# Kernel tuning notes

Hardware: AMD Instinct MI355X
Metric: run time of the kernel (lower is better)

The kernel has to match this reference:

```python
import jax, jax.numpy as jnp
import numpy as np

EMBED_DIM = 768
NUM_HEADS = 12
HEAD_DIM = EMBED_DIM // NUM_HEADS
B, T = 2, 2048


def setup_inputs() -> dict:
    key = jax.random.key(0)
    kx, kq, kqb, ko, kob = jax.random.split(key, 5)
    x = jax.random.normal(kx, (B, T, EMBED_DIM), dtype=jnp.float32)
    # xavier-uniform style params
    lim_qkv = float(np.sqrt(6.0 / (EMBED_DIM + 3 * EMBED_DIM)))
    qkv_kernel = jax.random.uniform(kq, (EMBED_DIM, 3 * EMBED_DIM), minval=-lim_qkv, maxval=lim_qkv, dtype=jnp.float32)
    qkv_bias = jnp.zeros((3 * EMBED_DIM,), dtype=jnp.float32)
    lim_o = float(np.sqrt(6.0 / (EMBED_DIM + EMBED_DIM)))
    o_kernel = jax.random.uniform(ko, (EMBED_DIM, EMBED_DIM), minval=-lim_o, maxval=lim_o, dtype=jnp.float32)
    o_bias = jnp.zeros((EMBED_DIM,), dtype=jnp.float32)
    return {"x": x, "qkv_kernel": qkv_kernel, "qkv_bias": qkv_bias, "o_kernel": o_kernel, "o_bias": o_bias}


def reference(x, qkv_kernel, qkv_bias, o_kernel, o_bias):
    b, t, d = x.shape
    # fused QKV projection
    qkv = jnp.einsum('btd,de->bte', x, qkv_kernel) + qkv_bias  # [B,T,3D]
    qkv = qkv.reshape(b, t, 3, NUM_HEADS, HEAD_DIM).transpose(2, 0, 3, 1, 4)  # [3,B,H,T,Dh]
    q, k, v = qkv[0], qkv[1], qkv[2]
    # naive attention: materializes full [B,H,T,T] scores (as in original)
    scale = 1.0 / np.sqrt(HEAD_DIM).astype(np.float32)
    attn_logits = jnp.einsum('bhqd,bhkd->bhqk', q, k) * scale
    attention = jax.nn.softmax(attn_logits, axis=-1)
    values = jnp.einsum('bhqk,bhkd->bhqd', attention, v)
    values = values.transpose(0, 2, 1, 3).reshape(b, t, d)  # [B,T,D]
    o = jnp.einsum('btd,de->bte', values, o_kernel) + o_bias
    return (o, attention)
```

## Files before the change

### kernel.cpp

```cpp
#include <hip/hip_runtime.h>
#include <hip/hip_bf16.h>
#include <hip/hip_fp16.h>

typedef _Float16 f16;
typedef _Float16 f16x4 __attribute__((ext_vector_type(4)));
typedef _Float16 f16x8 __attribute__((ext_vector_type(8)));
typedef float f32x4 __attribute__((ext_vector_type(4)));

#define MFMA16(a, b, c) __builtin_amdgcn_mfma_f32_16x16x32_f16(a, b, c, 0, 0, 0)

__device__ __forceinline__ float fexp2(float x) {
#if __has_builtin(__builtin_amdgcn_exp2f)
    return __builtin_amdgcn_exp2f(x);
#else
    return exp2f(x);
#endif
}

typedef __attribute__((address_space(1))) const void gconst_t;
typedef __attribute__((address_space(3))) void lds_t;
__device__ __forceinline__ void gload16(const f16* g, f16* l) {
    __builtin_amdgcn_global_load_lds((gconst_t*)g, (lds_t*)l, 16, 0, 0);
}

__global__ void k_convert_x(const float* __restrict__ in, f16* __restrict__ out, int n4) {
    int i = blockIdx.x * blockDim.x + threadIdx.x;
    if (i >= n4) return;
    float4 v = ((const float4*)in)[i];
    f16x4 o = {(f16)v.x, (f16)v.y, (f16)v.z, (f16)v.w};
    ((f16x4*)out)[i] = o;
}

__global__ __launch_bounds__(256) void k_transpose(const float* __restrict__ in,
                                                   f16* __restrict__ out, int K, int N) {
    __shared__ f16 tile[64][72];
    int n0 = blockIdx.x * 64, k0 = blockIdx.y * 64;
    int t = threadIdx.x;
    int r = t >> 2, cb = (t & 3) * 16;
    const float* src = in + (size_t)(k0 + r) * N + n0 + cb;
#pragma unroll
    for (int j = 0; j < 4; ++j) {
        float4 v = ((const float4*)src)[j];
        tile[r][cb + 4 * j + 0] = (f16)v.x;
        tile[r][cb + 4 * j + 1] = (f16)v.y;
        tile[r][cb + 4 * j + 2] = (f16)v.z;
        tile[r][cb + 4 * j + 3] = (f16)v.w;
    }
    __syncthreads();
    int nl = t >> 2, kb = (t & 3) * 16;
    f16* dst = out + (size_t)(n0 + nl) * K + k0 + kb;
#pragma unroll
    for (int j = 0; j < 2; ++j) {
        f16x8 o;
#pragma unroll
        for (int e = 0; e < 8; ++e) o[e] = tile[kb + 8 * j + e][nl];
        *(f16x8*)(dst + 8 * j) = o;
    }
}

__device__ __forceinline__ void gemm_core(const f16* __restrict__ A, const f16* __restrict__ Bt,
                                          int m0, int n0, int lane, int w, int wr, int wc,
                                          f16* As, f16* Bs, f32x4 acc[4][4]) {
    int prow = lane >> 2, pc = lane & 3;
    int lrow = prow ^ ((prow >> 2) & 1);
    int lcol = (pc ^ (lrow & 3)) * 8;
    int rsw = (lane & 7) << 3;
    for (int kt = 0; kt < 24; ++kt) {
        const f16* ab = A + (size_t)(m0 + w * 32 + lrow) * 768 + kt * 32 + lcol;
        const f16* bb = Bt + (size_t)(n0 + w * 32 + lrow) * 768 + kt * 32 + lcol;
        gload16(ab, As + (w * 32) * 32);
        gload16(ab + (size_t)16 * 768, As + (w * 32 + 16) * 32);
        gload16(bb, Bs + (w * 32) * 32);
        gload16(bb + (size_t)16 * 768, Bs + (w * 32 + 16) * 32);
        __syncthreads();
        f16x8 a[4], b[4];
#pragma unroll
        for (int i = 0; i < 4; ++i) {
            int idx = (wr * 64 + i * 16 + (lane & 15)) * 32 + (lane >> 4) * 8;
            a[i] = *(const f16x8*)(As + (idx ^ rsw));
        }
#pragma unroll
        for (int j = 0; j < 4; ++j) {
            int idx = (wc * 64 + j * 16 + (lane & 15)) * 32 + (lane >> 4) * 8;
            b[j] = *(const f16x8*)(Bs + (idx ^ rsw));
        }
#pragma unroll
        for (int i = 0; i < 4; ++i)
#pragma unroll
            for (int j = 0; j < 4; ++j) acc[i][j] = MFMA16(a[i], b[j], acc[i][j]);
        __syncthreads();
    }
}

__global__ __launch_bounds__(256) void k_qkv_gemm(const f16* __restrict__ A, const f16* __restrict__ Bt,
                                                  const float* __restrict__ bias,
                                                  f16* __restrict__ Qh, f16* __restrict__ Kf,
                                                  f16* __restrict__ Vf) {
    __shared__ __align__(16) f16 As[128 * 32];
    __shared__ __align__(16) f16 Bs[128 * 32];
    int m0 = blockIdx.x * 128, n0 = blockIdx.y * 128;
    int t = threadIdx.x, lane = t & 63, w = t >> 6;
    int wr = w >> 1, wc = w & 1;
    f32x4 zero = {0.f, 0.f, 0.f, 0.f};
    f32x4 acc[4][4];
#pragma unroll
    for (int i = 0; i < 4; ++i)
#pragma unroll
        for (int j = 0; j < 4; ++j) acc[i][j] = zero;

    gemm_core(A, Bt, m0, n0, lane, w, wr, wc, As, Bs, acc);

    const float QSCALE = 0.18033688011112042f;
#pragma unroll
    for (int j = 0; j < 4; ++j) {
        int n = n0 + wc * 64 + j * 16 + (lane & 15);
        int which = n / 768;
        int rem = n - which * 768;
        int h = rem >> 6, d = rem & 63;
        float bv = bias[n];
#pragma unroll
        for (int i = 0; i < 4; ++i) {
            int m = m0 + wr * 64 + i * 16 + ((lane >> 4) << 2);
            int bb = m >> 11, tt = m & 2047;
            int bh = bb * 12 + h;
            if (which == 2) {
                int kt = tt >> 6;
                int half = (tt & 63) >> 5, hi = (tt & 31) >> 3, e0 = tt & 7;
                int jd = d >> 4, lo = d & 15;
                size_t addr = (((size_t)bh * 32 + kt) * 8 + jd * 2 + half) * 512 +
                              (size_t)(hi * 16 + lo) * 8 + e0;
                f16x4 pk;
#pragma unroll
                for (int r = 0; r < 4; ++r) pk[r] = (f16)(acc[i][j][r] + bv);
                *(f16x4*)(Vf + addr) = pk;
            } else if (which == 0) {
#pragma unroll
                for (int r = 0; r < 4; ++r)
                    Qh[((size_t)bh * 2048 + tt + r) * 64 + d] = (f16)((acc[i][j][r] + bv) * QSCALE);
            } else {
                int half = d >> 5, hi = (d & 31) >> 3, e = d & 7;
#pragma unroll
                for (int r = 0; r < 4; ++r) {
                    int tr = tt + r;
                    int kt = tr >> 6, row = tr & 63;
                    int s = row >> 4, lo = row & 15;
                    size_t addr = (((size_t)bh * 32 + kt) * 8 + s * 2 + half) * 512 +
                                  (size_t)(hi * 16 + lo) * 8 + e;
                    Kf[addr] = (f16)(acc[i][j][r] + bv);
                }
            }
        }
    }
}

__global__ __launch_bounds__(256) void k_o_gemm(const f16* __restrict__ A, const f16* __restrict__ Bt,
                                                const float* __restrict__ bias,
                                                float* __restrict__ out) {
    __shared__ __align__(16) f16 As[128 * 32];
    __shared__ __align__(16) f16 Bs[128 * 32];
    int m0 = blockIdx.x * 128, n0 = blockIdx.y * 128;
    int t = threadIdx.x, lane = t & 63, w = t >> 6;
    int wr = w >> 1, wc = w & 1;
    f32x4 zero = {0.f, 0.f, 0.f, 0.f};
    f32x4 acc[4][4];
#pragma unroll
    for (int i = 0; i < 4; ++i)
#pragma unroll
        for (int j = 0; j < 4; ++j) acc[i][j] = zero;

    gemm_core(A, Bt, m0, n0, lane, w, wr, wc, As, Bs, acc);

#pragma unroll
    for (int j = 0; j < 4; ++j) {
        int n = n0 + wc * 64 + j * 16 + (lane & 15);
        float bv = bias[n];
#pragma unroll
        for (int i = 0; i < 4; ++i) {
            int m = m0 + wr * 64 + i * 16 + ((lane >> 4) << 2);
#pragma unroll
            for (int r = 0; r < 4; ++r) out[(size_t)(m + r) * 768 + n] = acc[i][j][r] + bv;
        }
    }
}

__global__ __launch_bounds__(256) void k_lsum(const f16* __restrict__ Qh, const f16* __restrict__ Kf,
                                              float* __restrict__ lpart) {
    int qt = blockIdx.x, bh = blockIdx.y, kc = blockIdx.z;
    int q0 = qt * 64;
    int t = threadIdx.x, lane = t & 63, w = t >> 6;
    const f16* qbase = Qh + ((size_t)bh * 2048 + q0 + w * 16) * 64;
    const f16* kfb = Kf + (size_t)bh * 32 * 4096 + (size_t)lane * 8;

    f16x8 aq[2];
#pragma unroll
    for (int f = 0; f < 2; ++f)
        aq[f] = *(const f16x8*)(qbase + (size_t)(lane & 15) * 64 + f * 32 + (lane >> 4) * 8);
    f32x4 zero = {0.f, 0.f, 0.f, 0.f};

    auto LOADK = [&](f16x8* dst, int kt) {
        const f16* kp = kfb + (size_t)kt * 4096;
#pragma unroll
        for (int f = 0; f < 8; ++f) dst[f] = *(const f16x8*)(kp + f * 512);
    };
    auto QKTS = [&](const f16x8* kf, f32x4* s4) {
#pragma unroll
        for (int s = 0; s < 4; ++s) {
            s4[s] = MFMA16(kf[2 * s], aq[0], zero);
            s4[s] = MFMA16(kf[2 * s + 1], aq[1], s4[s]);
        }
    };

    f16x8 ka[8], kb2[8];
    float lsum = 0.f;
    int base = kc * 8;
    LOADK(ka, base);
    for (int i = 0; i < 8; i += 2) {
        f32x4 s4[4];
        LOADK(kb2, base + i + 1);
        QKTS(ka, s4);
#pragma unroll
        for (int s = 0; s < 4; ++s)
#pragma unroll
            for (int r = 0; r < 4; ++r) lsum += fexp2(s4[s][r]);
        LOADK(ka, base + ((i + 2) & 7));
        QKTS(kb2, s4);
#pragma unroll
        for (int s = 0; s < 4; ++s)
#pragma unroll
            for (int r = 0; r < 4; ++r) lsum += fexp2(s4[s][r]);
    }
    lsum += __shfl_xor(lsum, 16, 64);
    lsum += __shfl_xor(lsum, 32, 64);
    float* lp = lpart + (size_t)kc * 49152 + (size_t)bh * 2048 + q0 + w * 16;
    if (lane < 16) lp[lane] = lsum;
}

__global__ __launch_bounds__(512, 4) void k_attn(const f16* __restrict__ Qh, const f16* __restrict__ Kf,
                                                 const f16* __restrict__ Vf,
                                                 const float* __restrict__ lpart,
                                                 float* __restrict__ attn, f16* __restrict__ valh) {
    __shared__ __align__(16) float Ps32_all[8][16 * 68];
    int orig = blockIdx.x;
    int swz = (orig & 7) * 96 + (orig >> 3);
    int bh = swz >> 5, qt = swz & 31;
    int q0 = qt * 64;
    int t = threadIdx.x, lane = t & 63, w = t >> 6;
    int qg = w >> 1, half = w & 1;

    const f16* qbase = Qh + ((size_t)bh * 2048 + q0 + qg * 16) * 64;
    const f16* kfb = Kf + (size_t)bh * 32 * 4096 + (size_t)lane * 8;
    const f16* vfb = Vf + (size_t)bh * 32 * 4096 + (size_t)lane * 8;

    f16x8 aq[2];
#pragma unroll
    for (int f = 0; f < 2; ++f)
        aq[f] = *(const f16x8*)(qbase + (size_t)(lane & 15) * 64 + f * 32 + (lane >> 4) * 8);
    f32x4 zero = {0.f, 0.f, 0.f, 0.f};

    float linv;
    {
        size_t qoff = (size_t)bh * 2048 + q0 + qg * 16 + (lane & 15);
        float s = 0.f;
#pragma unroll
        for (int kc = 0; kc < 4; ++kc) s += lpart[(size_t)kc * 49152 + qoff];
        linv = 1.0f / s;
    }

    auto LOADK = [&](f16x8* dst, int kt) {
        const f16* kp = kfb + (size_t)kt * 4096;
#pragma unroll
        for (int f = 0; f < 8; ++f) dst[f] = *(const f16x8*)(kp + f * 512);
    };

    f32x4 accv[4];
#pragma unroll
    for (int j = 0; j < 4; ++j) accv[j] = zero;
    float* Ps = Ps32_all[w];
    float* attn_base = attn + ((size_t)bh * 2048 + q0 + qg * 16) * 2048;
    f16x8 ka[8], vbuf[8];

    int ktbase = half * 16;
    LOADK(ka, ktbase);
    for (int kt = ktbase; kt < ktbase + 16; ++kt) {
        {
            const f16* vp = vfb + (size_t)kt * 4096;
#pragma unroll
            for (int f = 0; f < 8; ++f) vbuf[f] = *(const f16x8*)(vp + f * 512);
        }
        f32x4 s4[4];
#pragma unroll
        for (int s = 0; s < 4; ++s) {
            s4[s] = MFMA16(ka[2 * s], aq[0], zero);
            s4[s] = MFMA16(ka[2 * s + 1], aq[1], s4[s]);
        }
        LOADK(ka, (kt + 1) & 31);
#pragma unroll
        for (int s = 0; s < 4; ++s) {
            f32x4 pv;
#pragma unroll
            for (int r = 0; r < 4; ++r) pv[r] = fexp2(s4[s][r]) * linv;
            *(f32x4*)(Ps + (lane & 15) * 68 + s * 16 + (lane >> 4) * 4) = pv;
        }
        f16x8 pa[2];
#pragma unroll
        for (int hh = 0; hh < 2; ++hh) {
            const float* pr = Ps + (lane & 15) * 68 + hh * 32 + (lane >> 4) * 8;
            f32x4 lo = *(const f32x4*)(pr);
            f32x4 hi = *(const f32x4*)(pr + 4);
            f16x8 pf = {(f16)lo[0], (f16)lo[1], (f16)lo[2], (f16)lo[3],
                        (f16)hi[0], (f16)hi[1], (f16)hi[2], (f16)hi[3]};
            pa[hh] = pf;
        }
        float* ab = attn_base + kt * 64;
#pragma unroll
        for (int i = 0; i < 4; ++i) {
            int row = i * 4 + (lane >> 4);
            int col = (lane & 15) * 4;
            f32x4 v = *(const f32x4*)(Ps + row * 68 + col);
            *(f32x4*)(ab + (size_t)row * 2048 + col) = v;
        }
#pragma unroll
        for (int jd = 0; jd < 4; ++jd) {
            accv[jd] = MFMA16(pa[0], vbuf[2 * jd], accv[jd]);
            accv[jd] = MFMA16(pa[1], vbuf[2 * jd + 1], accv[jd]);
        }
    }

    if (half) {
#pragma unroll
        for (int j = 0; j < 4; ++j)
#pragma unroll
            for (int r = 0; r < 4; ++r)
                Ps[((lane >> 4) * 4 + r) * 68 + j * 16 + (lane & 15)] = accv[j][r];
    }
    __syncthreads();
    if (!half) {
        const float* Pp = Ps32_all[w + 1];
        int b = bh / 12, h = bh - b * 12;
#pragma unroll
        for (int j = 0; j < 4; ++j) {
#pragma unroll
            for (int r = 0; r < 4; ++r) {
                float v = accv[j][r] + Pp[((lane >> 4) * 4 + r) * 68 + j * 16 + (lane & 15)];
                int rowg = b * 2048 + q0 + qg * 16 + (lane >> 4) * 4 + r;
                int col = h * 64 + j * 16 + (lane & 15);
                valh[(size_t)rowg * 768 + col] = (f16)v;
            }
        }
    }
}

extern "C" void kernel_launch(void* const* d_in, const int* in_sizes, int n_in,
                              void* d_out, int out_size, void* d_ws, size_t ws_size,
                              hipStream_t stream) {
    const float* x = (const float*)d_in[0];
    const float* wqkv = (const float*)d_in[1];
    const float* bqkv = (const float*)d_in[2];
    const float* wo = (const float*)d_in[3];
    const float* bo = (const float*)d_in[4];

    float* out_o = (float*)d_out;
    float* out_attn = out_o + (size_t)2 * 2048 * 768;

    f16* ws = (f16*)d_ws;
    f16* xh = ws;
    f16* wqkv_t = xh + 3145728;
    f16* wo_t = wqkv_t + 1769472;
    f16* Qh = wo_t + 589824;
    f16* Kf = Qh + 3145728;
    f16* Vf = Kf + 3145728;
    f16* valh = Vf + 3145728;
    float* lpart = (float*)(valh + 3145728);

    k_convert_x<<<3072, 256, 0, stream>>>(x, xh, 786432);
    k_transpose<<<dim3(36, 12), 256, 0, stream>>>(wqkv, wqkv_t, 768, 2304);
    k_transpose<<<dim3(12, 12), 256, 0, stream>>>(wo, wo_t, 768, 768);
    k_qkv_gemm<<<dim3(32, 18), 256, 0, stream>>>(xh, wqkv_t, bqkv, Qh, Kf, Vf);
    k_lsum<<<dim3(32, 24, 4), 256, 0, stream>>>(Qh, Kf, lpart);
    k_attn<<<768, 512, 0, stream>>>(Qh, Kf, Vf, lpart, out_attn, valh);
    k_o_gemm<<<dim3(32, 6), 256, 0, stream>>>(valh, wo_t, bo, out_o);
}
```

Baseline: 200.0 us.

## Software-pipeline attention loop with double-buffered LDS probability tile

Restructures the k_attn inner loop into a one-stage software pipeline. Each iteration computes QK^T and exp for tile kt into one LDS buffer while reading the previous tile's probabilities from a second buffer for the attention store and the PV MFMA. This decouples the LDS write-read dependency within an iteration so MFMA, LDS and global traffic can overlap. In exchange LDS use per block doubles, which may limit occupancy at 4 blocks per CU, and the prologue and epilogue add code.

After: 216.1 us. 1.08x slower.

```diff
diff --git a/kernel.cpp b/kernel.cpp
--- a/kernel.cpp
+++ b/kernel.cpp
@@ -239,7 +239,7 @@
                                                  const f16* __restrict__ Vf,
                                                  const float* __restrict__ lpart,
                                                  float* __restrict__ attn, f16* __restrict__ valh) {
-    __shared__ __align__(16) float Ps32_all[8][16 * 68];
+    __shared__ __align__(16) float Ps32_all[8][2][16 * 68];
     int orig = blockIdx.x;
     int swz = (orig & 7) * 96 + (orig >> 3);
     int bh = swz >> 5, qt = swz & 31;
@@ -266,34 +266,25 @@
         linv = 1.0f / s;
     }
 
-    auto LOADK = [&](f16x8* dst, int kt) {
+    f16x8 ka[8], vbuf[8];
+    auto LOADK = [&](int kt) {
         const f16* kp = kfb + (size_t)kt * 4096;
 #pragma unroll
-        for (int f = 0; f < 8; ++f) dst[f] = *(const f16x8*)(kp + f * 512);
-    };
-
-    f32x4 accv[4];
-#pragma unroll
-    for (int j = 0; j < 4; ++j) accv[j] = zero;
-    float* Ps = Ps32_all[w];
-    float* attn_base = attn + ((size_t)bh * 2048 + q0 + qg * 16) * 2048;
-    f16x8 ka[8], vbuf[8];
-
-    int ktbase = half * 16;
-    LOADK(ka, ktbase);
-    for (int kt = ktbase; kt < ktbase + 16; ++kt) {
-        {
-            const f16* vp = vfb + (size_t)kt * 4096;
-#pragma unroll
-            for (int f = 0; f < 8; ++f) vbuf[f] = *(const f16x8*)(vp + f * 512);
-        }
-        f32x4 s4[4];
+        for (int f = 0; f < 8; ++f) ka[f] = *(const f16x8*)(kp + f * 512);
+    };
+    auto LOADV = [&](int kt) {
+        const f16* vp = vfb + (size_t)kt * 4096;
+#pragma unroll
+        for (int f = 0; f < 8; ++f) vbuf[f] = *(const f16x8*)(vp + f * 512);
+    };
+    auto QKTS = [&](f32x4* s4) {
 #pragma unroll
         for (int s = 0; s < 4; ++s) {
             s4[s] = MFMA16(ka[2 * s], aq[0], zero);
             s4[s] = MFMA16(ka[2 * s + 1], aq[1], s4[s]);
         }
-        LOADK(ka, (kt + 1) & 31);
+    };
+    auto WRITEPS = [&](float* Ps, f32x4* s4) {
 #pragma unroll
         for (int s = 0; s < 4; ++s) {
             f32x4 pv;
@@ -301,41 +292,93 @@
             for (int r = 0; r < 4; ++r) pv[r] = fexp2(s4[s][r]) * linv;
             *(f32x4*)(Ps + (lane & 15) * 68 + s * 16 + (lane >> 4) * 4) = pv;
         }
-        f16x8 pa[2];
-#pragma unroll
-        for (int hh = 0; hh < 2; ++hh) {
-            const float* pr = Ps + (lane & 15) * 68 + hh * 32 + (lane >> 4) * 8;
-            f32x4 lo = *(const f32x4*)(pr);
-            f32x4 hi = *(const f32x4*)(pr + 4);
-            f16x8 pf = {(f16)lo[0], (f16)lo[1], (f16)lo[2], (f16)lo[3],
-                        (f16)hi[0], (f16)hi[1], (f16)hi[2], (f16)hi[3]};
-            pa[hh] = pf;
-        }
-        float* ab = attn_base + kt * 64;
-#pragma unroll
-        for (int i = 0; i < 4; ++i) {
-            int row = i * 4 + (lane >> 4);
-            int col = (lane & 15) * 4;
-            f32x4 v = *(const f32x4*)(Ps + row * 68 + col);
-            *(f32x4*)(ab + (size_t)row * 2048 + col) = v;
-        }
+    };
+
+    f32x4 accv[4];
+#pragma unroll
+    for (int j = 0; j < 4; ++j) accv[j] = zero;
+    float* PsW = Ps32_all[w][0];
+    float* PsR = Ps32_all[w][1];
+    float* attn_base = attn + ((size_t)bh * 2048 + q0 + qg * 16) * 2048;
+
+    int ktbase = half * 16;
+    LOADK(ktbase);
+    {
+        f32x4 s4[4];
+        QKTS(s4);
+        LOADK(ktbase + 1);
+        WRITEPS(PsW, s4);
+        float* tmp = PsW; PsW = PsR; PsR = tmp;
+    }
+    for (int i = 1; i < 16; ++i) {
+        int kt = ktbase + i, ktp = kt - 1;
+        LOADV(ktp);
+        const float* pr0 = PsR + (lane & 15) * 68 + (lane >> 4) * 8;
+        f32x4 plo0 = *(const f32x4*)(pr0);
+        f32x4 phi0 = *(const f32x4*)(pr0 + 4);
+        f32x4 plo1 = *(const f32x4*)(pr0 + 32);
+        f32x4 phi1 = *(const f32x4*)(pr0 + 36);
+        f32x4 s4[4];
+        QKTS(s4);
+        LOADK((kt + 1) & 31);
+        f32x4 srow[4];
+#pragma unroll
+        for (int ii = 0; ii < 4; ++ii)
+            srow[ii] = *(const f32x4*)(PsR + (ii * 4 + (lane >> 4)) * 68 + (lane & 15) * 4);
+        WRITEPS(PsW, s4);
+        float* ab = attn_base + ktp * 64;
+#pragma unroll
+        for (int ii = 0; ii < 4; ++ii)
+            *(f32x4*)(ab + (size_t)(ii * 4 + (lane >> 4)) * 2048 + (lane & 15) * 4) = srow[ii];
+        f16x8 pa0 = {(f16)plo0[0], (f16)plo0[1], (f16)plo0[2], (f16)plo0[3],
+                     (f16)phi0[0], (f16)phi0[1], (f16)phi0[2], (f16)phi0[3]};
+        f16x8 pa1 = {(f16)plo1[0], (f16)plo1[1], (f16)plo1[2], (f16)plo1[3],
+                     (f16)phi1[0], (f16)phi1[1], (f16)phi1[2], (f16)phi1[3]};
 #pragma unroll
         for (int jd = 0; jd < 4; ++jd) {
-            accv[jd] = MFMA16(pa[0], vbuf[2 * jd], accv[jd]);
-            accv[jd] = MFMA16(pa[1], vbuf[2 * jd + 1], accv[jd]);
-        }
-    }
-
+            accv[jd] = MFMA16(pa0, vbuf[2 * jd], accv[jd]);
+            accv[jd] = MFMA16(pa1, vbuf[2 * jd + 1], accv[jd]);
+        }
+        float* tmp = PsW; PsW = PsR; PsR = tmp;
+    }
+    {
+        int ktp = ktbase + 15;
+        LOADV(ktp);
+        const float* pr0 = PsR + (lane & 15) * 68 + (lane >> 4) * 8;
+        f32x4 plo0 = *(const f32x4*)(pr0);
+        f32x4 phi0 = *(const f32x4*)(pr0 + 4);
+        f32x4 plo1 = *(const f32x4*)(pr0 + 32);
+        f32x4 phi1 = *(const f32x4*)(pr0 + 36);
+        f32x4 srow[4];
+#pragma unroll
+        for (int ii = 0; ii < 4; ++ii)
+            srow[ii] = *(const f32x4*)(PsR + (ii * 4 + (lane >> 4)) * 68 + (lane & 15) * 4);
+        float* ab = attn_base + ktp * 64;
+#pragma unroll
+        for (int ii = 0; ii < 4; ++ii)
+            *(f32x4*)(ab + (size_t)(ii * 4 + (lane >> 4)) * 2048 + (lane & 15) * 4) = srow[ii];
+        f16x8 pa0 = {(f16)plo0[0], (f16)plo0[1], (f16)plo0[2], (f16)plo0[3],
+                     (f16)phi0[0], (f16)phi0[1], (f16)phi0[2], (f16)phi0[3]};
+        f16x8 pa1 = {(f16)plo1[0], (f16)plo1[1], (f16)plo1[2], (f16)plo1[3],
+                     (f16)phi1[0], (f16)phi1[1], (f16)phi1[2], (f16)phi1[3]};
+#pragma unroll
+        for (int jd = 0; jd < 4; ++jd) {
+            accv[jd] = MFMA16(pa0, vbuf[2 * jd], accv[jd]);
+            accv[jd] = MFMA16(pa1, vbuf[2 * jd + 1], accv[jd]);
+        }
+    }
+
+    float* Pc = Ps32_all[w][0];
     if (half) {
 #pragma unroll
         for (int j = 0; j < 4; ++j)
 #pragma unroll
             for (int r = 0; r < 4; ++r)
-                Ps[((lane >> 4) * 4 + r) * 68 + j * 16 + (lane & 15)] = accv[j][r];
+                Pc[((lane >> 4) * 4 + r) * 68 + j * 16 + (lane & 15)] = accv[j][r];
     }
     __syncthreads();
     if (!half) {
-        const float* Pp = Ps32_all[w + 1];
+        const float* Pp = Ps32_all[w + 1][0];
         int b = bh / 12, h = bh - b * 12;
 #pragma unroll
         for (int j = 0; j < 4; ++j) {
```
